# Kernel tuning notes

Measured on AMD Instinct MI355X. Metric: run time of the kernel, lower is better.

## Reference

```python
import jax, jax.numpy as jnp
import numpy as np

B, N, DIM = 4, 8192, 512
HEADS, DIM_HEAD = 8, 64
INNER = HEADS * DIM_HEAD
SCALE = DIM_HEAD ** -0.5


def setup_inputs() -> dict:
    key = jax.random.key(0)
    ks = jax.random.split(key, 8)
    return {
        "x": jax.random.normal(ks[0], (B, N, DIM), jnp.float32),
        "mask": jnp.zeros((B, N), jnp.bool_),
        "W_qkv": jax.random.normal(ks[1], (3 * INNER, DIM), jnp.float32) * 0.02,
        "w_q_logits": jax.random.normal(ks[2], (DIM_HEAD,), jnp.float32) * 0.02,
        "w_k_logits": jax.random.normal(ks[3], (DIM_HEAD,), jnp.float32) * 0.02,
        "W_r": jax.random.normal(ks[4], (DIM_HEAD, DIM_HEAD), jnp.float32) * 0.02,
        "b_r": jnp.zeros((DIM_HEAD,), jnp.float32),
        "W_out": jax.random.normal(ks[5], (DIM, INNER), jnp.float32) * 0.02,
        "b_out": jnp.zeros((DIM,), jnp.float32),
    }


def reference(x, mask, W_qkv, w_q_logits, w_k_logits, W_r, b_r, W_out, b_out):
    b, n, _ = x.shape
    neg_inf = jnp.float32(-jnp.inf)
    qkv = x @ W_qkv.T                              # (b, n, 3*inner)
    q, k, v = jnp.split(qkv, 3, axis=-1)           # each (b, n, inner)
    # faithful to torch: contiguous().view(b, heads, n, dim_head) == plain reshape
    q = q.reshape(b, HEADS, n, DIM_HEAD)
    k = k.reshape(b, HEADS, n, DIM_HEAD)
    v = v.reshape(b, HEADS, n, DIM_HEAD)
    m = mask[:, None, :]                           # (b, 1, n)

    # query pooling -> global query vector
    q_logits = jnp.einsum('bhnd,d->bhn', q, w_q_logits) * SCALE
    q_attn = jax.nn.softmax(jnp.where(m, neg_inf, q_logits), axis=-1)
    global_q = jnp.einsum('bhn,bhnd->bhd', q_attn, q)   # (b, h, d)

    # gate keys with global query, pool -> global key vector
    kg = k * global_q[:, :, None, :]
    k_logits = jnp.einsum('bhnd,d->bhn', kg, w_k_logits) * SCALE
    k_attn = jax.nn.softmax(jnp.where(m, neg_inf, k_logits), axis=-1)
    global_k = jnp.einsum('bhn,bhnd->bhd', k_attn, k)   # pools original k (k_agg)

    # gate values with global key, project, residual with q
    vg = v * global_k[:, :, None, :]
    r = vg @ W_r.T + b_r + q                            # (b, h, n, d)
    r = r.reshape(b, n, INNER)
    return r @ W_out.T + b_out
```

## Files before the change

kernel.cpp:

```cpp
#include <hip/hip_runtime.h>
#include <cstdint>

#define NB    4
#define NSEQ  8192
#define NDIM  512
#define NHEAD 8
#define DH    64
#define NTOK  (NB * NSEQ)
#define QKV_W 1536
#define SCALE 0.125f

typedef unsigned short u16;
typedef __attribute__((ext_vector_type(8))) unsigned short u16x8;
typedef __attribute__((ext_vector_type(4))) unsigned short u16x4;
typedef __attribute__((ext_vector_type(8))) short s16x8;
typedef __attribute__((ext_vector_type(4))) float f32x4;

__device__ __forceinline__ float bf2f(u16 u) {
  return __uint_as_float(((unsigned int)u) << 16);
}
__device__ __forceinline__ u16 f2bf(float f) {
  unsigned int x = __float_as_uint(f);
  x += 0x7fffu + ((x >> 16) & 1u);
  return (u16)(x >> 16);
}
__device__ __forceinline__ void gload_lds16(const void* g, void* l) {
  __builtin_amdgcn_global_load_lds(
      (const __attribute__((address_space(1))) unsigned int*)g,
      (__attribute__((address_space(3))) unsigned int*)l, 16, 0, 0);
}

__global__ __launch_bounds__(256) void cvt_bf16(
    const float* __restrict__ s0, u16* __restrict__ d0, int n0,
    const float* __restrict__ s1, u16* __restrict__ d1, int n1,
    const float* __restrict__ s2, u16* __restrict__ d2, int n2) {
  int gid = blockIdx.x * 256 + threadIdx.x;
  int stride = gridDim.x * 256;
  int t0 = n0 >> 2, t1 = n1 >> 2, t2 = n2 >> 2;
  for (int i = gid; i < t0; i += stride) {
    f32x4 v = ((const f32x4*)s0)[i];
    u16x4 o; o[0]=f2bf(v[0]); o[1]=f2bf(v[1]); o[2]=f2bf(v[2]); o[3]=f2bf(v[3]);
    ((u16x4*)d0)[i] = o;
  }
  for (int i = gid; i < t1; i += stride) {
    f32x4 v = ((const f32x4*)s1)[i];
    u16x4 o; o[0]=f2bf(v[0]); o[1]=f2bf(v[1]); o[2]=f2bf(v[2]); o[3]=f2bf(v[3]);
    ((u16x4*)d1)[i] = o;
  }
  for (int i = gid; i < t2; i += stride) {
    f32x4 v = ((const f32x4*)s2)[i];
    u16x4 o; o[0]=f2bf(v[0]); o[1]=f2bf(v[1]); o[2]=f2bf(v[2]); o[3]=f2bf(v[3]);
    ((u16x4*)d2)[i] = o;
  }
}

__global__ __launch_bounds__(512, 2) void gemm256(
    const u16* __restrict__ A, const u16* __restrict__ B,
    int K, int tiles_n,
    u16* __restrict__ Cbf, float* __restrict__ Cf,
    const float* __restrict__ bias) {
  __shared__ u16 lds[65536];
  const int KT = K >> 6;

  const int nwg = gridDim.x, bid = blockIdx.x;
  const int cpx = nwg >> 3;
  const int swz = (bid & 7) * cpx + (bid >> 3);
  const int tm = swz / tiles_n, tn = swz - tm * tiles_n;

  const int tid = threadIdx.x, lane = tid & 63, wid = tid >> 6;
  const int wm = wid >> 2, wn = wid & 3;
  const int rA = lane & 15, kq = lane >> 4, swl = lane & 7;

  const u16* Ab = A + (size_t)tm * 256 * K;
  const u16* Bb = B + (size_t)tn * 256 * K;

  auto STAGE = [&](int isB, int d, int h, int kt) {
    const u16* src = isB ? Bb : Ab;
    const int base = (isB ? 32768 : 0) + (d * 2 + h) * 8192;
#pragma unroll
    for (int r = 0; r < 2; ++r) {
      const int slot = r * 512 + tid;
      const int row = slot >> 3, ch = slot & 7;
      gload_lds16(src + (size_t)(h * 128 + row) * K + kt * 64 +
                      ((ch ^ (row & 7)) << 3),
                  &lds[base + slot * 8]);
    }
  };

  f32x4 acc[8][4] = {};

  STAGE(0, 0, 0, 0); STAGE(0, 0, 1, 0);
  STAGE(1, 0, 0, 0); STAGE(1, 0, 1, 0);
  {
    const int k1 = (KT > 1) ? 1 : 0;
    STAGE(1, 1, 0, k1); STAGE(1, 1, 1, k1);
  }
  asm volatile("s_waitcnt vmcnt(4)" ::: "memory");
  __builtin_amdgcn_s_barrier();

#define LDA(m, kk) (*(const s16x8*)&lds[Abase + ((m) * 16 + rA) * 64 + \
                                        ((((kk) * 4 + kq) ^ swl) << 3)])
#define LDB(n, kk) (*(const s16x8*)&lds[Bbase + (brow + (n) * 16 + rA) * 64 + \
                                        ((((kk) * 4 + kq) ^ swl) << 3)])
#define MFMA_(a, b, c) __builtin_amdgcn_mfma_f32_16x16x32_bf16(a, b, c, 0, 0, 0)

#define PHASE(M0, M1, BREAD, STG, TAIL)                                  \
  {                                                                      \
    s16x8 a00 = LDA(M0, 0), a01 = LDA(M0, 1);                            \
    s16x8 a10 = LDA(M1, 0), a11 = LDA(M1, 1);                            \
    BREAD                                                                \
    STG                                                                  \
    __builtin_amdgcn_s_barrier();                                        \
    asm volatile("s_waitcnt lgkmcnt(0)" ::: "memory");                   \
    __builtin_amdgcn_s_setprio(1);                                       \
    acc[M0][0] = MFMA_(a00, b00, acc[M0][0]);                            \
    acc[M0][0] = MFMA_(a01, b01, acc[M0][0]);                            \
    acc[M0][1] = MFMA_(a00, b10, acc[M0][1]);                            \
    acc[M0][1] = MFMA_(a01, b11, acc[M0][1]);                            \
    acc[M0][2] = MFMA_(a00, b20, acc[M0][2]);                            \
    acc[M0][2] = MFMA_(a01, b21, acc[M0][2]);                            \
    acc[M0][3] = MFMA_(a00, b30, acc[M0][3]);                            \
    acc[M0][3] = MFMA_(a01, b31, acc[M0][3]);                            \
    acc[M1][0] = MFMA_(a10, b00, acc[M1][0]);                            \
    acc[M1][0] = MFMA_(a11, b01, acc[M1][0]);                            \
    acc[M1][1] = MFMA_(a10, b10, acc[M1][1]);                            \
    acc[M1][1] = MFMA_(a11, b11, acc[M1][1]);                            \
    acc[M1][2] = MFMA_(a10, b20, acc[M1][2]);                            \
    acc[M1][2] = MFMA_(a11, b21, acc[M1][2]);                            \
    acc[M1][3] = MFMA_(a10, b30, acc[M1][3]);                            \
    acc[M1][3] = MFMA_(a11, b31, acc[M1][3]);                            \
    __builtin_amdgcn_s_setprio(0);                                       \
    TAIL                                                                 \
    __builtin_amdgcn_s_barrier();                                        \
  }

  for (int t = 0; t < KT; ++t) {
    const int d = t & 1;
    const int kA = (t + 1 < KT) ? t + 1 : KT - 1;
    const int kB = (t + 2 < KT) ? t + 2 : KT - 1;
    const int Abase = (d * 2 + wm) * 8192;
    const int Bbase = 32768 + (d * 2 + (wn >> 1)) * 8192;
    const int brow = (wn & 1) * 64;

    s16x8 b00, b01, b10, b11, b20, b21, b30, b31;

    PHASE(0, 1,
          { b00 = LDB(0, 0); b01 = LDB(0, 1); b10 = LDB(1, 0); b11 = LDB(1, 1);
            b20 = LDB(2, 0); b21 = LDB(2, 1); b30 = LDB(3, 0); b31 = LDB(3, 1); },
          STAGE(0, d ^ 1, 0, kA);, )
    PHASE(2, 3, , STAGE(0, d ^ 1, 1, kA);, )
    PHASE(4, 5, , STAGE(1, d, 0, kB);, )
    PHASE(6, 7, , STAGE(1, d, 1, kB);,
          asm volatile("s_waitcnt vmcnt(4)" ::: "memory");)
  }

  asm volatile("s_waitcnt vmcnt(0)" ::: "memory");

  const int crow = kq * 4;
  const int ccol = rA;
  const size_t row_base = (size_t)tm * 256 + wm * 128;
  const int col_base = tn * 256 + wn * 64;
  const int N = tiles_n << 8;
  if (Cbf) {
#pragma unroll
    for (int m = 0; m < 8; ++m)
#pragma unroll
      for (int n = 0; n < 4; ++n)
#pragma unroll
        for (int j = 0; j < 4; ++j)
          Cbf[(row_base + m * 16 + crow + j) * N + col_base + n * 16 + ccol] =
              f2bf(acc[m][n][j]);
  } else {
#pragma unroll
    for (int m = 0; m < 8; ++m)
#pragma unroll
      for (int n = 0; n < 4; ++n) {
        int col = col_base + n * 16 + ccol;
        float bv = bias[col];
#pragma unroll
        for (int j = 0; j < 4; ++j)
          Cf[(row_base + m * 16 + crow + j) * N + col] = acc[m][n][j] + bv;
      }
  }
#undef LDA
#undef LDB
#undef MFMA_
#undef PHASE
}

__global__ __launch_bounds__(256) void pool_stage(
    const u16* __restrict__ qkv, int chan_off,
    const float* __restrict__ wvec, float scale,
    float* __restrict__ partS, float* __restrict__ partG) {
  __shared__ float redG[4][64];
  __shared__ float redS[4];
  const int bid = blockIdx.x;
  const int bh = bid >> 3, chunk = bid & 7;
  const int b = bh >> 3, h = bh & 7;
  const int tid = threadIdx.x, lane = tid & 63, w = tid >> 6;
  const int j = lane & 7;

  float wreg[8];
#pragma unroll
  for (int i = 0; i < 8; ++i) wreg[i] = wvec[j * 8 + i];

  float accS = 0.f;
  float accG[8] = {};
  const size_t tok0 = (size_t)b * NSEQ + (size_t)h * 1024 + chunk * 128;

  for (int it = 0; it < 32; ++it) {
    const u16* row = qkv + (tok0 + it * 4 + w) * QKV_W + chan_off;
    u16x8 q8 = *(const u16x8*)(row + lane * 8);
    float qf[8];
#pragma unroll
    for (int i = 0; i < 8; ++i) qf[i] = bf2f(q8[i]);
    float dot = 0.f;
#pragma unroll
    for (int i = 0; i < 8; ++i) dot += qf[i] * wreg[i];
    dot += __shfl_xor(dot, 1);
    dot += __shfl_xor(dot, 2);
    dot += __shfl_xor(dot, 4);
    float e = __expf(dot * scale);
    accS += (j == 0) ? e : 0.f;
#pragma unroll
    for (int i = 0; i < 8; ++i) accG[i] += e * qf[i];
  }
#pragma unroll
  for (int m = 8; m <= 32; m <<= 1) {
    accS += __shfl_xor(accS, m);
#pragma unroll
    for (int i = 0; i < 8; ++i) accG[i] += __shfl_xor(accG[i], m);
  }
  if (lane < 8) {
#pragma unroll
    for (int i = 0; i < 8; ++i) redG[w][lane * 8 + i] = accG[i];
    if (lane == 0) redS[w] = accS;
  }
  __syncthreads();
  if (tid < 64) {
    float G = redG[0][tid] + redG[1][tid] + redG[2][tid] + redG[3][tid];
    partG[(size_t)bid * 64 + tid] = G;
    if (tid == 0) partS[bid] = redS[0] + redS[1] + redS[2] + redS[3];
  }
}

__global__ __launch_bounds__(64) void finalize_pool(
    const float* __restrict__ partS, const float* __restrict__ partG,
    const float* __restrict__ mulvec, float scale,
    float* __restrict__ outv) {
  int bh = blockIdx.x, d = threadIdx.x;
  float S = 0.f, G = 0.f;
#pragma unroll
  for (int c = 0; c < 8; ++c) {
    S += partS[bh * 8 + c];
    G += partG[(bh * 8 + c) * 64 + d];
  }
  float g = G / S;
  if (mulvec) g *= mulvec[d] * scale;
  outv[bh * 64 + d] = g;
}

__global__ __launch_bounds__(256) void weff_prep(
    const float* __restrict__ Wr, const float* __restrict__ gk,
    u16* __restrict__ weff) {
  const int bh = blockIdx.x, tid = threadIdx.x;
  for (int i = tid; i < 4096; i += 256) {
    int e = i & 63;
    weff[bh * 4096 + i] = f2bf(Wr[i] * gk[bh * 64 + e]);
  }
}

__global__ __launch_bounds__(256) void r_mfma(
    const u16* __restrict__ qkv, const u16* __restrict__ weff,
    const float* __restrict__ b_r, u16* __restrict__ rout) {
  const int tid = threadIdx.x, lane = tid & 63, wv = tid >> 6;
  const size_t rho0 = (size_t)blockIdx.x * 256 + wv * 64;
  const int bh = (int)(rho0 >> 13);
  const int rA = lane & 15, kq = lane >> 4;

#define MFMA_(a, b, c) __builtin_amdgcn_mfma_f32_16x16x32_bf16(a, b, c, 0, 0, 0)

  s16x8 af[4][2];
  const u16* wb = weff + bh * 4096;
#pragma unroll
  for (int fm = 0; fm < 4; ++fm)
#pragma unroll
    for (int kk = 0; kk < 2; ++kk)
      af[fm][kk] = *(const s16x8*)(wb + (fm * 16 + rA) * 64 + kk * 32 + kq * 8);

  f32x4 br4[4];
#pragma unroll
  for (int fm = 0; fm < 4; ++fm)
    br4[fm] = *(const f32x4*)(b_r + fm * 16 + kq * 4);

  f32x4 acc[4][4] = {};
#pragma unroll
  for (int fn = 0; fn < 4; ++fn) {
    const size_t rho = rho0 + fn * 16 + rA;
    const u16* vr = qkv + (rho >> 3) * QKV_W + 1024 + (rho & 7) * 64;
    s16x8 b0 = *(const s16x8*)(vr + kq * 8);
    s16x8 b1 = *(const s16x8*)(vr + 32 + kq * 8);
#pragma unroll
    for (int fm = 0; fm < 4; ++fm) {
      acc[fm][fn] = MFMA_(af[fm][0], b0, acc[fm][fn]);
      acc[fm][fn] = MFMA_(af[fm][1], b1, acc[fm][fn]);
    }
  }

#pragma unroll
  for (int fn = 0; fn < 4; ++fn) {
    const size_t rho = rho0 + fn * 16 + rA;
    const size_t t = rho >> 3;
    const int g = (int)(rho & 7);
    const u16* qr = qkv + t * QKV_W + g * 64;
    u16* orow = rout + t * NDIM + g * 64;
#pragma unroll
    for (int fm = 0; fm < 4; ++fm) {
      const int d0 = fm * 16 + kq * 4;
      u16x4 q4 = *(const u16x4*)(qr + d0);
      u16x4 o;
#pragma unroll
      for (int j = 0; j < 4; ++j)
        o[j] = f2bf(acc[fm][fn][j] + br4[fm][j] + bf2f(q4[j]));
      *(u16x4*)(orow + d0) = o;
    }
  }
#undef MFMA_
}

extern "C" void kernel_launch(void* const* d_in, const int* in_sizes, int n_in,
                              void* d_out, int out_size, void* d_ws,
                              size_t ws_size, hipStream_t stream) {
  const float* x    = (const float*)d_in[0];
  const float* Wqkv = (const float*)d_in[2];
  const float* wq   = (const float*)d_in[3];
  const float* wk   = (const float*)d_in[4];
  const float* Wr   = (const float*)d_in[5];
  const float* br   = (const float*)d_in[6];
  const float* Wout = (const float*)d_in[7];
  const float* bout = (const float*)d_in[8];
  float* out = (float*)d_out;

  char* w = (char*)d_ws;
  auto carve = [&](size_t bytes) {
    char* p = w;
    w += (bytes + 255) & ~(size_t)255;
    return p;
  };
  u16* x_bf    = (u16*)carve((size_t)NTOK * NDIM * 2);
  u16* qkv_bf  = (u16*)carve((size_t)NTOK * QKV_W * 2);
  u16* Wqkv_bf = (u16*)carve((size_t)QKV_W * NDIM * 2);
  u16* Wout_bf = (u16*)carve((size_t)NDIM * NDIM * 2);
  float* partS  = (float*)carve(256 * 4);
  float* partG  = (float*)carve(256 * 64 * 4);
  float* wk_eff = (float*)carve(32 * 64 * 4);
  float* gk     = (float*)carve(32 * 64 * 4);
  u16* weff    = (u16*)carve(32 * 64 * 64 * 2);
  u16* r_bf    = x_bf;

  cvt_bf16<<<2048, 256, 0, stream>>>(x, x_bf, NTOK * NDIM,
                                     Wqkv, Wqkv_bf, QKV_W * NDIM,
                                     Wout, Wout_bf, NDIM * NDIM);
  gemm256<<<128 * 6, 512, 0, stream>>>(x_bf, Wqkv_bf, NDIM, 6,
                                       qkv_bf, nullptr, nullptr);
  pool_stage<<<256, 256, 0, stream>>>(qkv_bf, 0, wq, SCALE, partS, partG);
  finalize_pool<<<32, 64, 0, stream>>>(partS, partG, wk, SCALE, wk_eff);
  pool_stage<<<256, 256, 0, stream>>>(qkv_bf, 512, wk_eff, 1.0f, partS, partG);
  finalize_pool<<<32, 64, 0, stream>>>(partS, partG, nullptr, 1.0f, gk);
  weff_prep<<<32, 256, 0, stream>>>(Wr, gk, weff);
  r_mfma<<<NTOK * 8 / 256, 256, 0, stream>>>(qkv_bf, weff, br, r_bf);
  gemm256<<<128 * 2, 512, 0, stream>>>(r_bf, Wout_bf, NDIM, 2,
                                       nullptr, out, bout);
}
```

Measured before the change: 274.7 us.

## Halve GEMM K-tile to raise occupancy and split pooling into more blocks

The GEMM K-step drops from 64 to 32, which halves LDS use to 64KB. Launch bounds rise to 4 blocks per CU, and the LDS swizzle and phase schedule are restructured into two halves per K-step. The pooling stage is split into 1024 blocks instead of 256, with finalize summing 32 partials, so more CUs can pull memory bandwidth. The trade-off is twice as many barriers and loop iterations in the GEMM, and possible register spills under the tighter occupancy bound.

```diff
diff --git a/kernel.cpp b/kernel.cpp
--- a/kernel.cpp
+++ b/kernel.cpp
@@ -54,13 +54,13 @@
   }
 }
 
-__global__ __launch_bounds__(512, 2) void gemm256(
+__global__ __launch_bounds__(512, 4) void gemm256(
     const u16* __restrict__ A, const u16* __restrict__ B,
     int K, int tiles_n,
     u16* __restrict__ Cbf, float* __restrict__ Cf,
     const float* __restrict__ bias) {
-  __shared__ u16 lds[65536];
-  const int KT = K >> 6;
+  __shared__ u16 lds[32768];
+  const int KT = K >> 5;
 
   const int nwg = gridDim.x, bid = blockIdx.x;
   const int cpx = nwg >> 3;
@@ -69,22 +69,20 @@
 
   const int tid = threadIdx.x, lane = tid & 63, wid = tid >> 6;
   const int wm = wid >> 2, wn = wid & 3;
-  const int rA = lane & 15, kq = lane >> 4, swl = lane & 7;
+  const int rA = lane & 15, kq = lane >> 4;
+  const int swl = (rA >> 1) & 3;
+  const int co = (kq ^ swl) << 3;
 
   const u16* Ab = A + (size_t)tm * 256 * K;
   const u16* Bb = B + (size_t)tn * 256 * K;
 
   auto STAGE = [&](int isB, int d, int h, int kt) {
     const u16* src = isB ? Bb : Ab;
-    const int base = (isB ? 32768 : 0) + (d * 2 + h) * 8192;
-#pragma unroll
-    for (int r = 0; r < 2; ++r) {
-      const int slot = r * 512 + tid;
-      const int row = slot >> 3, ch = slot & 7;
-      gload_lds16(src + (size_t)(h * 128 + row) * K + kt * 64 +
-                      ((ch ^ (row & 7)) << 3),
-                  &lds[base + slot * 8]);
-    }
+    const int base = (isB ? 16384 : 0) + (d * 2 + h) * 4096;
+    const int row = tid >> 2, ch = tid & 3;
+    gload_lds16(src + (size_t)(h * 128 + row) * K + kt * 32 +
+                    ((ch ^ ((row >> 1) & 3)) << 3),
+                &lds[base + tid * 8]);
   };
 
   f32x4 acc[8][4] = {};
@@ -95,63 +93,75 @@
     const int k1 = (KT > 1) ? 1 : 0;
     STAGE(1, 1, 0, k1); STAGE(1, 1, 1, k1);
   }
-  asm volatile("s_waitcnt vmcnt(4)" ::: "memory");
+  asm volatile("s_waitcnt vmcnt(2)" ::: "memory");
   __builtin_amdgcn_s_barrier();
 
-#define LDA(m, kk) (*(const s16x8*)&lds[Abase + ((m) * 16 + rA) * 64 + \
-                                        ((((kk) * 4 + kq) ^ swl) << 3)])
-#define LDB(n, kk) (*(const s16x8*)&lds[Bbase + (brow + (n) * 16 + rA) * 64 + \
-                                        ((((kk) * 4 + kq) ^ swl) << 3)])
+#define LDA(m) (*(const s16x8*)&lds[Abase + ((m) * 16 + rA) * 32 + co])
+#define LDB(n) (*(const s16x8*)&lds[Bbase + (brow + (n) * 16 + rA) * 32 + co])
 #define MFMA_(a, b, c) __builtin_amdgcn_mfma_f32_16x16x32_bf16(a, b, c, 0, 0, 0)
-
-#define PHASE(M0, M1, BREAD, STG, TAIL)                                  \
-  {                                                                      \
-    s16x8 a00 = LDA(M0, 0), a01 = LDA(M0, 1);                            \
-    s16x8 a10 = LDA(M1, 0), a11 = LDA(M1, 1);                            \
-    BREAD                                                                \
-    STG                                                                  \
-    __builtin_amdgcn_s_barrier();                                        \
-    asm volatile("s_waitcnt lgkmcnt(0)" ::: "memory");                   \
-    __builtin_amdgcn_s_setprio(1);                                       \
-    acc[M0][0] = MFMA_(a00, b00, acc[M0][0]);                            \
-    acc[M0][0] = MFMA_(a01, b01, acc[M0][0]);                            \
-    acc[M0][1] = MFMA_(a00, b10, acc[M0][1]);                            \
-    acc[M0][1] = MFMA_(a01, b11, acc[M0][1]);                            \
-    acc[M0][2] = MFMA_(a00, b20, acc[M0][2]);                            \
-    acc[M0][2] = MFMA_(a01, b21, acc[M0][2]);                            \
-    acc[M0][3] = MFMA_(a00, b30, acc[M0][3]);                            \
-    acc[M0][3] = MFMA_(a01, b31, acc[M0][3]);                            \
-    acc[M1][0] = MFMA_(a10, b00, acc[M1][0]);                            \
-    acc[M1][0] = MFMA_(a11, b01, acc[M1][0]);                            \
-    acc[M1][1] = MFMA_(a10, b10, acc[M1][1]);                            \
-    acc[M1][1] = MFMA_(a11, b11, acc[M1][1]);                            \
-    acc[M1][2] = MFMA_(a10, b20, acc[M1][2]);                            \
-    acc[M1][2] = MFMA_(a11, b21, acc[M1][2]);                            \
-    acc[M1][3] = MFMA_(a10, b30, acc[M1][3]);                            \
-    acc[M1][3] = MFMA_(a11, b31, acc[M1][3]);                            \
-    __builtin_amdgcn_s_setprio(0);                                       \
-    TAIL                                                                 \
-    __builtin_amdgcn_s_barrier();                                        \
-  }
 
   for (int t = 0; t < KT; ++t) {
     const int d = t & 1;
     const int kA = (t + 1 < KT) ? t + 1 : KT - 1;
     const int kB = (t + 2 < KT) ? t + 2 : KT - 1;
-    const int Abase = (d * 2 + wm) * 8192;
-    const int Bbase = 32768 + (d * 2 + (wn >> 1)) * 8192;
+    const int Abase = (d * 2 + wm) * 4096;
+    const int Bbase = 16384 + (d * 2 + (wn >> 1)) * 4096;
     const int brow = (wn & 1) * 64;
 
-    s16x8 b00, b01, b10, b11, b20, b21, b30, b31;
-
-    PHASE(0, 1,
-          { b00 = LDB(0, 0); b01 = LDB(0, 1); b10 = LDB(1, 0); b11 = LDB(1, 1);
-            b20 = LDB(2, 0); b21 = LDB(2, 1); b30 = LDB(3, 0); b31 = LDB(3, 1); },
-          STAGE(0, d ^ 1, 0, kA);, )
-    PHASE(2, 3, , STAGE(0, d ^ 1, 1, kA);, )
-    PHASE(4, 5, , STAGE(1, d, 0, kB);, )
-    PHASE(6, 7, , STAGE(1, d, 1, kB);,
-          asm volatile("s_waitcnt vmcnt(4)" ::: "memory");)
+    s16x8 b0, b1, b2, b3;
+
+    {
+      s16x8 a0 = LDA(0), a1 = LDA(1), a2 = LDA(2), a3 = LDA(3);
+      b0 = LDB(0); b1 = LDB(1); b2 = LDB(2); b3 = LDB(3);
+      STAGE(0, d ^ 1, 0, kA); STAGE(0, d ^ 1, 1, kA);
+      __builtin_amdgcn_s_barrier();
+      asm volatile("s_waitcnt lgkmcnt(0)" ::: "memory");
+      __builtin_amdgcn_s_setprio(1);
+      acc[0][0] = MFMA_(a0, b0, acc[0][0]);
+      acc[0][1] = MFMA_(a0, b1, acc[0][1]);
+      acc[0][2] = MFMA_(a0, b2, acc[0][2]);
+      acc[0][3] = MFMA_(a0, b3, acc[0][3]);
+      acc[1][0] = MFMA_(a1, b0, acc[1][0]);
+      acc[1][1] = MFMA_(a1, b1, acc[1][1]);
+      acc[1][2] = MFMA_(a1, b2, acc[1][2]);
+      acc[1][3] = MFMA_(a1, b3, acc[1][3]);
+      acc[2][0] = MFMA_(a2, b0, acc[2][0]);
+      acc[2][1] = MFMA_(a2, b1, acc[2][1]);
+      acc[2][2] = MFMA_(a2, b2, acc[2][2]);
+      acc[2][3] = MFMA_(a2, b3, acc[2][3]);
+      acc[3][0] = MFMA_(a3, b0, acc[3][0]);
+      acc[3][1] = MFMA_(a3, b1, acc[3][1]);
+      acc[3][2] = MFMA_(a3, b2, acc[3][2]);
+      acc[3][3] = MFMA_(a3, b3, acc[3][3]);
+      __builtin_amdgcn_s_setprio(0);
+      __builtin_amdgcn_s_barrier();
+    }
+    {
+      s16x8 a4 = LDA(4), a5 = LDA(5), a6 = LDA(6), a7 = LDA(7);
+      STAGE(1, d, 0, kB); STAGE(1, d, 1, kB);
+      __builtin_amdgcn_s_barrier();
+      asm volatile("s_waitcnt lgkmcnt(0)" ::: "memory");
+      __builtin_amdgcn_s_setprio(1);
+      acc[4][0] = MFMA_(a4, b0, acc[4][0]);
+      acc[4][1] = MFMA_(a4, b1, acc[4][1]);
+      acc[4][2] = MFMA_(a4, b2, acc[4][2]);
+      acc[4][3] = MFMA_(a4, b3, acc[4][3]);
+      acc[5][0] = MFMA_(a5, b0, acc[5][0]);
+      acc[5][1] = MFMA_(a5, b1, acc[5][1]);
+      acc[5][2] = MFMA_(a5, b2, acc[5][2]);
+      acc[5][3] = MFMA_(a5, b3, acc[5][3]);
+      acc[6][0] = MFMA_(a6, b0, acc[6][0]);
+      acc[6][1] = MFMA_(a6, b1, acc[6][1]);
+      acc[6][2] = MFMA_(a6, b2, acc[6][2]);
+      acc[6][3] = MFMA_(a6, b3, acc[6][3]);
+      acc[7][0] = MFMA_(a7, b0, acc[7][0]);
+      acc[7][1] = MFMA_(a7, b1, acc[7][1]);
+      acc[7][2] = MFMA_(a7, b2, acc[7][2]);
+      acc[7][3] = MFMA_(a7, b3, acc[7][3]);
+      __builtin_amdgcn_s_setprio(0);
+      asm volatile("s_waitcnt vmcnt(2)" ::: "memory");
+      __builtin_amdgcn_s_barrier();
+    }
   }
 
   asm volatile("s_waitcnt vmcnt(0)" ::: "memory");
@@ -185,7 +195,6 @@
 #undef LDA
 #undef LDB
 #undef MFMA_
-#undef PHASE
 }
 
 __global__ __launch_bounds__(256) void pool_stage(
@@ -195,7 +204,7 @@
   __shared__ float redG[4][64];
   __shared__ float redS[4];
   const int bid = blockIdx.x;
-  const int bh = bid >> 3, chunk = bid & 7;
+  const int bh = bid >> 5, chunk = bid & 31;
   const int b = bh >> 3, h = bh & 7;
   const int tid = threadIdx.x, lane = tid & 63, w = tid >> 6;
   const int j = lane & 7;
@@ -206,9 +215,9 @@
 
   float accS = 0.f;
   float accG[8] = {};
-  const size_t tok0 = (size_t)b * NSEQ + (size_t)h * 1024 + chunk * 128;
-
-  for (int it = 0; it < 32; ++it) {
+  const size_t tok0 = (size_t)b * NSEQ + (size_t)h * 1024 + chunk * 32;
+
+  for (int it = 0; it < 8; ++it) {
     const u16* row = qkv + (tok0 + it * 4 + w) * QKV_W + chan_off;
     u16x8 q8 = *(const u16x8*)(row + lane * 8);
     float qf[8];
@@ -251,9 +260,9 @@
   int bh = blockIdx.x, d = threadIdx.x;
   float S = 0.f, G = 0.f;
 #pragma unroll
-  for (int c = 0; c < 8; ++c) {
-    S += partS[bh * 8 + c];
-    G += partG[(bh * 8 + c) * 64 + d];
+  for (int c = 0; c < 32; ++c) {
+    S += partS[bh * 32 + c];
+    G += partG[(size_t)(bh * 32 + c) * 64 + d];
   }
   float g = G / S;
   if (mulvec) g *= mulvec[d] * scale;
@@ -351,8 +360,8 @@
   u16* qkv_bf  = (u16*)carve((size_t)NTOK * QKV_W * 2);
   u16* Wqkv_bf = (u16*)carve((size_t)QKV_W * NDIM * 2);
   u16* Wout_bf = (u16*)carve((size_t)NDIM * NDIM * 2);
-  float* partS  = (float*)carve(256 * 4);
-  float* partG  = (float*)carve(256 * 64 * 4);
+  float* partS  = (float*)carve(1024 * 4);
+  float* partG  = (float*)carve(1024 * 64 * 4);
   float* wk_eff = (float*)carve(32 * 64 * 4);
   float* gk     = (float*)carve(32 * 64 * 4);
   u16* weff    = (u16*)carve(32 * 64 * 64 * 2);
@@ -363,9 +372,9 @@
                                      Wout, Wout_bf, NDIM * NDIM);
   gemm256<<<128 * 6, 512, 0, stream>>>(x_bf, Wqkv_bf, NDIM, 6,
                                        qkv_bf, nullptr, nullptr);
-  pool_stage<<<256, 256, 0, stream>>>(qkv_bf, 0, wq, SCALE, partS, partG);
+  pool_stage<<<1024, 256, 0, stream>>>(qkv_bf, 0, wq, SCALE, partS, partG);
   finalize_pool<<<32, 64, 0, stream>>>(partS, partG, wk, SCALE, wk_eff);
-  pool_stage<<<256, 256, 0, stream>>>(qkv_bf, 512, wk_eff, 1.0f, partS, partG);
+  pool_stage<<<1024, 256, 0, stream>>>(qkv_bf, 512, wk_eff, 1.0f, partS, partG);
   finalize_pool<<<32, 64, 0, stream>>>(partS, partG, nullptr, 1.0f, gk);
   weff_prep<<<32, 256, 0, stream>>>(Wr, gk, weff);
   r_mfma<<<NTOK * 8 / 256, 256, 0, stream>>>(qkv_bf, weff, br, r_bf);
```

After: 907.8 us. 3.3x slower.

## Fuse pool finalization and weight prep into consumer kernels, widen pooling grid

Applied to the files above, without the earlier changes.

Removes the two finalize_pool kernels and weff_prep. Each consumer block now reduces the partial sums itself: pool_k builds the gated key weight vector, and r_mfma computes the global key and forms the scaled W_r fragments in registers. The pooling kernels also go from 256 to 1024 blocks, each covering 32 tokens, to occupy more CUs. This cuts three launches and their serial dependencies, but every block repeats a small 32-way reduction and r_mfma reads fp32 W_r directly instead of a prepared bf16 copy.

```diff
diff --git a/kernel.cpp b/kernel.cpp
--- a/kernel.cpp
+++ b/kernel.cpp
@@ -188,28 +188,27 @@
 #undef PHASE
 }
 
-__global__ __launch_bounds__(256) void pool_stage(
-    const u16* __restrict__ qkv, int chan_off,
-    const float* __restrict__ wvec, float scale,
+__global__ __launch_bounds__(256) void pool_q(
+    const u16* __restrict__ qkv, const float* __restrict__ wq,
     float* __restrict__ partS, float* __restrict__ partG) {
   __shared__ float redG[4][64];
   __shared__ float redS[4];
   const int bid = blockIdx.x;
-  const int bh = bid >> 3, chunk = bid & 7;
+  const int bh = bid >> 5, chunk = bid & 31;
   const int b = bh >> 3, h = bh & 7;
   const int tid = threadIdx.x, lane = tid & 63, w = tid >> 6;
   const int j = lane & 7;
 
   float wreg[8];
 #pragma unroll
-  for (int i = 0; i < 8; ++i) wreg[i] = wvec[j * 8 + i];
+  for (int i = 0; i < 8; ++i) wreg[i] = wq[j * 8 + i] * SCALE;
 
   float accS = 0.f;
   float accG[8] = {};
-  const size_t tok0 = (size_t)b * NSEQ + (size_t)h * 1024 + chunk * 128;
-
-  for (int it = 0; it < 32; ++it) {
-    const u16* row = qkv + (tok0 + it * 4 + w) * QKV_W + chan_off;
+  const size_t tok0 = (size_t)b * NSEQ + (size_t)h * 1024 + chunk * 32;
+
+  for (int it = 0; it < 8; ++it) {
+    const u16* row = qkv + (tok0 + it * 4 + w) * QKV_W;
     u16x8 q8 = *(const u16x8*)(row + lane * 8);
     float qf[8];
 #pragma unroll
@@ -220,7 +219,7 @@
     dot += __shfl_xor(dot, 1);
     dot += __shfl_xor(dot, 2);
     dot += __shfl_xor(dot, 4);
-    float e = __expf(dot * scale);
+    float e = __expf(dot);
     accS += (j == 0) ? e : 0.f;
 #pragma unroll
     for (int i = 0; i < 8; ++i) accG[i] += e * qf[i];
@@ -244,49 +243,110 @@
   }
 }
 
-__global__ __launch_bounds__(64) void finalize_pool(
-    const float* __restrict__ partS, const float* __restrict__ partG,
-    const float* __restrict__ mulvec, float scale,
-    float* __restrict__ outv) {
-  int bh = blockIdx.x, d = threadIdx.x;
-  float S = 0.f, G = 0.f;
-#pragma unroll
-  for (int c = 0; c < 8; ++c) {
-    S += partS[bh * 8 + c];
-    G += partG[(bh * 8 + c) * 64 + d];
-  }
-  float g = G / S;
-  if (mulvec) g *= mulvec[d] * scale;
-  outv[bh * 64 + d] = g;
-}
-
-__global__ __launch_bounds__(256) void weff_prep(
-    const float* __restrict__ Wr, const float* __restrict__ gk,
-    u16* __restrict__ weff) {
-  const int bh = blockIdx.x, tid = threadIdx.x;
-  for (int i = tid; i < 4096; i += 256) {
-    int e = i & 63;
-    weff[bh * 4096 + i] = f2bf(Wr[i] * gk[bh * 64 + e]);
+__global__ __launch_bounds__(256) void pool_k(
+    const u16* __restrict__ qkv,
+    const float* __restrict__ partSq, const float* __restrict__ partGq,
+    const float* __restrict__ wk,
+    float* __restrict__ partS, float* __restrict__ partG) {
+  __shared__ float redG[4][64];
+  __shared__ float redS[4];
+  __shared__ float wkl[64];
+  const int bid = blockIdx.x;
+  const int bh = bid >> 5, chunk = bid & 31;
+  const int b = bh >> 3, h = bh & 7;
+  const int tid = threadIdx.x, lane = tid & 63, w = tid >> 6;
+  const int j = lane & 7;
+
+  if (tid < 64) {
+    float S = 0.f, G = 0.f;
+#pragma unroll
+    for (int c = 0; c < 32; ++c) {
+      S += partSq[bh * 32 + c];
+      G += partGq[(size_t)(bh * 32 + c) * 64 + tid];
+    }
+    wkl[tid] = (G / S) * wk[tid] * SCALE;
+  }
+  __syncthreads();
+
+  float wreg[8];
+#pragma unroll
+  for (int i = 0; i < 8; ++i) wreg[i] = wkl[j * 8 + i];
+
+  float accS = 0.f;
+  float accG[8] = {};
+  const size_t tok0 = (size_t)b * NSEQ + (size_t)h * 1024 + chunk * 32;
+
+  for (int it = 0; it < 8; ++it) {
+    const u16* row = qkv + (tok0 + it * 4 + w) * QKV_W + 512;
+    u16x8 q8 = *(const u16x8*)(row + lane * 8);
+    float qf[8];
+#pragma unroll
+    for (int i = 0; i < 8; ++i) qf[i] = bf2f(q8[i]);
+    float dot = 0.f;
+#pragma unroll
+    for (int i = 0; i < 8; ++i) dot += qf[i] * wreg[i];
+    dot += __shfl_xor(dot, 1);
+    dot += __shfl_xor(dot, 2);
+    dot += __shfl_xor(dot, 4);
+    float e = __expf(dot);
+    accS += (j == 0) ? e : 0.f;
+#pragma unroll
+    for (int i = 0; i < 8; ++i) accG[i] += e * qf[i];
+  }
+#pragma unroll
+  for (int m = 8; m <= 32; m <<= 1) {
+    accS += __shfl_xor(accS, m);
+#pragma unroll
+    for (int i = 0; i < 8; ++i) accG[i] += __shfl_xor(accG[i], m);
+  }
+  if (lane < 8) {
+#pragma unroll
+    for (int i = 0; i < 8; ++i) redG[w][lane * 8 + i] = accG[i];
+    if (lane == 0) redS[w] = accS;
+  }
+  __syncthreads();
+  if (tid < 64) {
+    float G = redG[0][tid] + redG[1][tid] + redG[2][tid] + redG[3][tid];
+    partG[(size_t)bid * 64 + tid] = G;
+    if (tid == 0) partS[bid] = redS[0] + redS[1] + redS[2] + redS[3];
   }
 }
 
 __global__ __launch_bounds__(256) void r_mfma(
-    const u16* __restrict__ qkv, const u16* __restrict__ weff,
-    const float* __restrict__ b_r, u16* __restrict__ rout) {
+    const u16* __restrict__ qkv,
+    const float* __restrict__ partSk, const float* __restrict__ partGk,
+    const float* __restrict__ Wr, const float* __restrict__ b_r,
+    u16* __restrict__ rout) {
+  __shared__ float gkl[64];
   const int tid = threadIdx.x, lane = tid & 63, wv = tid >> 6;
   const size_t rho0 = (size_t)blockIdx.x * 256 + wv * 64;
   const int bh = (int)(rho0 >> 13);
   const int rA = lane & 15, kq = lane >> 4;
 
+  if (tid < 64) {
+    float S = 0.f, G = 0.f;
+#pragma unroll
+    for (int c = 0; c < 32; ++c) {
+      S += partSk[bh * 32 + c];
+      G += partGk[(size_t)(bh * 32 + c) * 64 + tid];
+    }
+    gkl[tid] = G / S;
+  }
+  __syncthreads();
+
 #define MFMA_(a, b, c) __builtin_amdgcn_mfma_f32_16x16x32_bf16(a, b, c, 0, 0, 0)
 
   s16x8 af[4][2];
-  const u16* wb = weff + bh * 4096;
 #pragma unroll
   for (int fm = 0; fm < 4; ++fm)
 #pragma unroll
-    for (int kk = 0; kk < 2; ++kk)
-      af[fm][kk] = *(const s16x8*)(wb + (fm * 16 + rA) * 64 + kk * 32 + kq * 8);
+    for (int kk = 0; kk < 2; ++kk) {
+      const int e0 = kk * 32 + kq * 8;
+      const float* wr = Wr + (fm * 16 + rA) * 64 + e0;
+#pragma unroll
+      for (int i = 0; i < 8; ++i)
+        af[fm][kk][i] = (short)f2bf(wr[i] * gkl[e0 + i]);
+    }
 
   f32x4 br4[4];
 #pragma unroll
@@ -351,11 +411,10 @@
   u16* qkv_bf  = (u16*)carve((size_t)NTOK * QKV_W * 2);
   u16* Wqkv_bf = (u16*)carve((size_t)QKV_W * NDIM * 2);
   u16* Wout_bf = (u16*)carve((size_t)NDIM * NDIM * 2);
-  float* partS  = (float*)carve(256 * 4);
-  float* partG  = (float*)carve(256 * 64 * 4);
-  float* wk_eff = (float*)carve(32 * 64 * 4);
-  float* gk     = (float*)carve(32 * 64 * 4);
-  u16* weff    = (u16*)carve(32 * 64 * 64 * 2);
+  float* partSq = (float*)carve(1024 * 4);
+  float* partGq = (float*)carve(1024 * 64 * 4);
+  float* partSk = (float*)carve(1024 * 4);
+  float* partGk = (float*)carve(1024 * 64 * 4);
   u16* r_bf    = x_bf;
 
   cvt_bf16<<<2048, 256, 0, stream>>>(x, x_bf, NTOK * NDIM,
@@ -363,12 +422,10 @@
                                      Wout, Wout_bf, NDIM * NDIM);
   gemm256<<<128 * 6, 512, 0, stream>>>(x_bf, Wqkv_bf, NDIM, 6,
                                        qkv_bf, nullptr, nullptr);
-  pool_stage<<<256, 256, 0, stream>>>(qkv_bf, 0, wq, SCALE, partS, partG);
-  finalize_pool<<<32, 64, 0, stream>>>(partS, partG, wk, SCALE, wk_eff);
-  pool_stage<<<256, 256, 0, stream>>>(qkv_bf, 512, wk_eff, 1.0f, partS, partG);
-  finalize_pool<<<32, 64, 0, stream>>>(partS, partG, nullptr, 1.0f, gk);
-  weff_prep<<<32, 256, 0, stream>>>(Wr, gk, weff);
-  r_mfma<<<NTOK * 8 / 256, 256, 0, stream>>>(qkv_bf, weff, br, r_bf);
+  pool_q<<<1024, 256, 0, stream>>>(qkv_bf, wq, partSq, partGq);
+  pool_k<<<1024, 256, 0, stream>>>(qkv_bf, partSq, partGq, wk, partSk, partGk);
+  r_mfma<<<NTOK * 8 / 256, 256, 0, stream>>>(qkv_bf, partSk, partGk, Wr, br,
+                                             r_bf);
   gemm256<<<128 * 2, 512, 0, stream>>>(r_bf, Wout_bf, NDIM, 2,
                                        nullptr, out, bout);
 }
```

New measurement: 265.1 us. 3.5% less time.
